# Kernel tuning notes

Hardware: AMD Instinct MI355X
Metric: run time of the kernel (lower is better)

## Reference

```python
import jax, jax.numpy as jnp
import numpy as np


def setup_inputs() -> dict:
    key = jax.random.key(0)
    ks = jax.random.split(key, 4)
    B, M, D = 512, 40, 64
    # split_half=True with layers [200,200,200]: prev = 40 -> 100 -> 100
    x = jax.random.normal(ks[0], (B, M, D), dtype=jnp.float32)
    w1 = jax.random.normal(ks[1], (200, M * 40), dtype=jnp.float32) * 0.02
    w2 = jax.random.normal(ks[2], (200, M * 100), dtype=jnp.float32) * 0.02
    w3 = jax.random.normal(ks[3], (200, M * 100), dtype=jnp.float32) * 0.02
    b1 = jnp.zeros((200,), dtype=jnp.float32)
    b2 = jnp.zeros((200,), dtype=jnp.float32)
    b3 = jnp.zeros((200,), dtype=jnp.float32)
    return {"x": x, "w1": w1, "b1": b1, "w2": w2, "b2": b2, "w3": w3, "b3": b3}


def reference(x, w1, b1, w2, b2, w3, b3):
    B, M, D = x.shape
    params = [(w1, b1), (w2, b2), (w3, b3)]
    n_layers = len(params)
    hidden = x  # (B, prev, D), starts as x0
    outs = []
    for i, (w, b) in enumerate(params):
        # outer product over field dims, flattened channel-major as in torch .view
        outer = jnp.einsum('bmd,bnd->bmnd', x, hidden).reshape(B, -1, D)
        # Conv1d kernel_size=1 == per-position linear over channels
        out = jax.nn.relu(jnp.einsum('bcd,oc->bod', outer, w) + b[None, :, None])
        if i < n_layers - 1:  # split_half
            half = out.shape[1] // 2
            out, direct = out[:, :half, :], out[:, half:, :]
            outs.append(direct)
        else:
            outs.append(out)
        hidden = out
    return jnp.concatenate(outs, axis=1).sum(axis=2)  # (B, 100+100+200)
```

## Files before the change

### kernel.cpp

```cpp
#include <hip/hip_runtime.h>
#include <hip/hip_bf16.h>


typedef float f32x4 __attribute__((ext_vector_type(4)));
typedef short bf16x8 __attribute__((ext_vector_type(8)));
typedef unsigned int uint;

#define XS_STR 44
#define HS_STR 108

struct LDSState {
    __hip_bfloat16 xs[2][64][XS_STR];
    __hip_bfloat16 hs[2][2][64][HS_STR];
    uint U[4][2][64][16];
};

static __device__ __forceinline__ float bflo(uint u) {
    uint v = u << 16; return __builtin_bit_cast(float, v);
}
static __device__ __forceinline__ float bfhi(uint u) {
    uint v = u & 0xffff0000u; return __builtin_bit_cast(float, v);
}
static __device__ __forceinline__ uint pk_bf16(float a, float b) {
    uint r; asm("v_cvt_pk_bf16_f32 %0, %1, %2" : "=v"(r) : "v"(a), "v"(b));
    return r;
}

#define PHASE_BAR() do {                                   \
    asm volatile("s_waitcnt lgkmcnt(0)" ::: "memory");     \
    __builtin_amdgcn_sched_barrier(0);                     \
    __builtin_amdgcn_s_barrier();                          \
    __builtin_amdgcn_sched_barrier(0);                     \
} while (0)

template<int DIV, int NK, int HASH, int ROWLO, int ROWOFF, int HSTR, int A>
__device__ __forceinline__ void layer_core(
    LDSState* L, const bf16x8* __restrict__ wpk, const float* __restrict__ bias,
    const __hip_bfloat16* __restrict__ h0, const __hip_bfloat16* __restrict__ h1,
    int dstpp, float* outb0, float* outb1, int tid, int mt0)
{
    const int lane = tid & 63;
    const int wv = tid >> 6, wn = wv & 1;
    const int q = lane >> 4, lr = lane & 15, d = lane;

    const int hdr = (lr >> 1) & 7;
    const uint* ub  = &L->U[0][0][0][0] + wn * 1024;
    const uint* roA = ub + (lr * 16 + 2 * ((2 * q) ^ hdr));
    const uint* roB = ub + (lr * 16 + 2 * ((2 * q + 1) ^ hdr));

    const int hdw = (d >> 1) & 7;
    uint* wb = &L->U[0][0][d][0] + 2 * (wv ^ hdw);

    const __hip_bfloat16* xb0 = &L->xs[0][d][0];
    const __hip_bfloat16* xb1 = &L->xs[1][d][0];
    const __hip_bfloat16* hb0 = h0 + d * HSTR;
    const __hip_bfloat16* hb1 = h1 + d * HSTR;

    f32x4 acc[A][4];
    #pragma unroll
    for (int mi = 0; mi < A; ++mi)
        #pragma unroll
        for (int nj = 0; nj < 4; ++nj)
            acc[mi][nj] = {0.f, 0.f, 0.f, 0.f};

    int bm = (4 * wv) / DIV;
    int bn = (4 * wv) % DIV;
    int bk = 0;
    auto build = [&]() {
        if (bk < NK) {
            const int slab_dw = (bk & 3) * 2048;
            float xf0 = __bfloat162float(xb0[bm]);
            float xf1 = __bfloat162float(xb1[bm]);
            uint2 ha = *(const uint2*)(hb0 + bn);
            uint2 hc = *(const uint2*)(hb1 + bn);
            uint2 w0, w1;
            w0.x = pk_bf16(xf0 * bflo(ha.x), xf0 * bfhi(ha.x));
            w0.y = pk_bf16(xf0 * bflo(ha.y), xf0 * bfhi(ha.y));
            w1.x = pk_bf16(xf1 * bflo(hc.x), xf1 * bfhi(hc.x));
            w1.y = pk_bf16(xf1 * bflo(hc.y), xf1 * bfhi(hc.y));
            *(uint2*)(wb + slab_dw)        = w0;
            *(uint2*)(wb + slab_dw + 1024) = w1;
            bn += 32;
            if (bn >= DIV) { bn -= DIV; ++bm; }
            ++bk;
        }
    };

    auto prefetch_bv = [&](int s1, bf16x8* bv) {
        const int slab_dw = (s1 & 3) * 2048;
        #pragma unroll
        for (int nj = 0; nj < 4; ++nj) {
            union { uint2 u2[2]; bf16x8 v; } t;
            t.u2[0] = *(const uint2*)(roA + slab_dw + nj * 256);
            t.u2[1] = *(const uint2*)(roB + slab_dw + nj * 256);
            bv[nj] = t.v;
        }
    };

    auto consume_regs = [&](bf16x8* f, bf16x8* bv) {
        #pragma unroll
        for (int mi = 0; mi < A; ++mi)
            #pragma unroll
            for (int nj = 0; nj < 4; ++nj)
                acc[mi][nj] = __builtin_amdgcn_mfma_f32_16x16x32_bf16(
                    f[mi], bv[nj], acc[mi][nj], 0, 0, 0);
    };

    const bf16x8* pw = wpk + (size_t)mt0 * NK * 64 + lane;
    auto loadf = [&](bf16x8* f, int s) {
        if (s < NK) {
            #pragma unroll
            for (int mi = 0; mi < A; ++mi)
                f[mi] = pw[(size_t)mi * NK * 64 + (size_t)s * 64];
        }
    };

    bf16x8 fC[A], fN[A], bvC[4], bvN[4];
    loadf(fC, 0); loadf(fN, 1);
    build(); build();
    __syncthreads();
    prefetch_bv(0, bvC);

    #pragma unroll 1
    for (int s = 0; s + 2 <= NK; s += 2) {
        prefetch_bv(s + 1, bvN);
        consume_regs(fC, bvC);
        loadf(fC, s + 2);
        build();
        PHASE_BAR();
        if (s + 2 < NK) prefetch_bv(s + 2, bvC);
        consume_regs(fN, bvN);
        loadf(fN, s + 3);
        build();
        PHASE_BAR();
    }
    if (NK & 1) consume_regs(fC, bvC);

    float* outp = wn ? outb1 : outb0;
    #pragma unroll
    for (int mi = 0; mi < A; ++mi) {
        const int mt = mt0 + mi;
        #pragma unroll
        for (int reg = 0; reg < 4; ++reg) {
            const int o = 16 * mt + 4 * q + reg;
            if (o < 200) {
                const float bs = bias[o];
                float r0 = fmaxf(acc[mi][0][reg] + bs, 0.f);
                float r1 = fmaxf(acc[mi][1][reg] + bs, 0.f);
                float r2 = fmaxf(acc[mi][2][reg] + bs, 0.f);
                float r3 = fmaxf(acc[mi][3][reg] + bs, 0.f);
                if (HASH && o < 100) {
                    L->hs[dstpp][wn][ 0 + lr][o] = __float2bfloat16(r0);
                    L->hs[dstpp][wn][16 + lr][o] = __float2bfloat16(r1);
                    L->hs[dstpp][wn][32 + lr][o] = __float2bfloat16(r2);
                    L->hs[dstpp][wn][48 + lr][o] = __float2bfloat16(r3);
                }
                if (o >= ROWLO) {
                    float sv = (r0 + r1) + (r2 + r3);
                    sv += __shfl_xor(sv, 1, 64);
                    sv += __shfl_xor(sv, 2, 64);
                    sv += __shfl_xor(sv, 4, 64);
                    sv += __shfl_xor(sv, 8, 64);
                    if (lr == 0) outp[ROWOFF + (o - ROWLO)] = sv;
                }
            }
        }
    }
    __syncthreads();
}

template<int A>
__device__ __forceinline__ void run_layers(
    LDSState* L, const bf16x8* w1p, const bf16x8* w2p, const bf16x8* w3p,
    const float* b1, const float* b2, const float* b3,
    float* outb0, float* outb1, int tid, int mt0)
{
    layer_core< 40,  50, 1, 100,   0, XS_STR, A>(L, w1p, b1,
        &L->xs[0][0][0], &L->xs[1][0][0], 0, outb0, outb1, tid, mt0);
    layer_core<100, 125, 1, 100, 100, HS_STR, A>(L, w2p, b2,
        &L->hs[0][0][0][0], &L->hs[0][1][0][0], 1, outb0, outb1, tid, mt0);
    layer_core<100, 125, 0,   0, 200, HS_STR, A>(L, w3p, b3,
        &L->hs[1][0][0][0], &L->hs[1][1][0][0], 0, outb0, outb1, tid, mt0);
}

__global__ __launch_bounds__(512, 2)
void fused_mfma(const float* __restrict__ x,
                const bf16x8* __restrict__ wpk,
                const float* __restrict__ b1, const float* __restrict__ b2,
                const float* __restrict__ b3, float* __restrict__ out) {
    __shared__ LDSState L;
    const int tid = threadIdx.x;
    const int bi  = blockIdx.x;

    const float* xg = x + (size_t)(2 * bi) * 2560;
    for (int i = tid; i < 5120; i += 512) {
        int bb = (i >= 2560) ? 1 : 0;
        int r  = i - bb * 2560;
        L.xs[bb][r & 63][r >> 6] = __float2bfloat16(xg[(size_t)bb * 2560 + r]);
    }
    __syncthreads();

    float* outb0 = out + (size_t)(2 * bi + 0) * 400;
    float* outb1 = out + (size_t)(2 * bi + 1) * 400;

    const bf16x8* w1p = wpk;
    const bf16x8* w2p = wpk + 41600;
    const bf16x8* w3p = wpk + 145600;

    const int wm = tid >> 7;
    if (wm == 0)
        run_layers<4>(&L, w1p, w2p, w3p, b1, b2, b3, outb0, outb1, tid, 0);
    else
        run_layers<3>(&L, w1p, w2p, w3p, b1, b2, b3, outb0, outb1, tid,
                      3 * wm + 1);
}

__global__ void convert_pack(const float* __restrict__ w1, const float* __restrict__ w2,
                             const float* __restrict__ w3, uint4* __restrict__ outp) {
    int c = blockIdx.x * 256 + threadIdx.x;
    if (c >= 249600) return;
    const float* src; int K, base;
    if (c < 41600)       { src = w1; K = 1600; base = c; }
    else if (c < 145600) { src = w2; K = 4000; base = c - 41600; }
    else                 { src = w3; K = 4000; base = c - 145600; }
    const int NS   = K / 32;
    const int lane = base & 63;
    const int t    = base >> 6;
    const int mt   = t / NS;
    const int s    = t - mt * NS;
    const int row  = 16 * mt + (lane & 15);
    const int k0   = 32 * s + 8 * (lane >> 4);
    uint o[4];
    if (row < 200) {
        const float* p = src + (size_t)row * K + k0;
        #pragma unroll
        for (int j = 0; j < 4; ++j) {
            __hip_bfloat16 lo = __float2bfloat16(p[2 * j]);
            __hip_bfloat16 hi = __float2bfloat16(p[2 * j + 1]);
            o[j] = (uint)__builtin_bit_cast(unsigned short, lo)
                 | ((uint)__builtin_bit_cast(unsigned short, hi) << 16);
        }
    } else {
        #pragma unroll
        for (int j = 0; j < 4; ++j) o[j] = 0u;
    }
    uint4 v; v.x = o[0]; v.y = o[1]; v.z = o[2]; v.w = o[3];
    outp[c] = v;
}

__global__ __launch_bounds__(512, 1)
void fused_bilinear_kernel(const float* __restrict__ x,
                           const float* __restrict__ w1, const float* __restrict__ b1,
                           const float* __restrict__ w2, const float* __restrict__ b2,
                           const float* __restrict__ w3, const float* __restrict__ b3,
                           float* __restrict__ out) {
    const int b   = blockIdx.x;
    const int tid = threadIdx.x;
    const int d   = tid & 63;
    const int wv  = tid >> 6;

    __shared__ float xs[40][64];
    __shared__ float hs[100][64];

    const float* xb = x + (size_t)b * 40 * 64;
    for (int i = tid; i < 40 * 64; i += 512) ((float*)xs)[i] = xb[i];
    __syncthreads();

    float xr[40];
    #pragma unroll
    for (int m = 0; m < 40; ++m) xr[m] = xs[m][d];
    float hr[100];
    const int o0 = __builtin_amdgcn_readfirstlane(wv * 25);

    for (int oi = 0; oi < 25; ++oi) {
        const int o = o0 + oi;
        const float* __restrict__ wrow = w1 + (size_t)o * 1600;
        float s = b1[o];
        for (int m = 0; m < 40; ++m) {
            const float* __restrict__ wm = wrow + m * 40;
            float a0 = 0.f, a1 = 0.f, a2 = 0.f, a3 = 0.f;
            #pragma unroll
            for (int n = 0; n < 40; n += 4) {
                a0 = fmaf(wm[n + 0], xr[n + 0], a0);
                a1 = fmaf(wm[n + 1], xr[n + 1], a1);
                a2 = fmaf(wm[n + 2], xr[n + 2], a2);
                a3 = fmaf(wm[n + 3], xr[n + 3], a3);
            }
            s = fmaf(xs[m][d], (a0 + a1) + (a2 + a3), s);
        }
        s = fmaxf(s, 0.f);
        if (o < 100) hs[o][d] = s;
        else {
            float r = s;
            #pragma unroll
            for (int off = 32; off > 0; off >>= 1) r += __shfl_xor(r, off, 64);
            if (d == 0) out[(size_t)b * 400 + (o - 100)] = r;
        }
    }
    __syncthreads();
    #pragma unroll
    for (int n = 0; n < 100; ++n) hr[n] = hs[n][d];
    __syncthreads();

    for (int oi = 0; oi < 25; ++oi) {
        const int o = o0 + oi;
        const float* __restrict__ wrow = w2 + (size_t)o * 4000;
        float s = b2[o];
        for (int m = 0; m < 40; ++m) {
            const float* __restrict__ wm = wrow + m * 100;
            float a0 = 0.f, a1 = 0.f, a2 = 0.f, a3 = 0.f;
            #pragma unroll
            for (int n = 0; n < 100; n += 4) {
                a0 = fmaf(wm[n + 0], hr[n + 0], a0);
                a1 = fmaf(wm[n + 1], hr[n + 1], a1);
                a2 = fmaf(wm[n + 2], hr[n + 2], a2);
                a3 = fmaf(wm[n + 3], hr[n + 3], a3);
            }
            s = fmaf(xs[m][d], (a0 + a1) + (a2 + a3), s);
        }
        s = fmaxf(s, 0.f);
        if (o < 100) hs[o][d] = s;
        else {
            float r = s;
            #pragma unroll
            for (int off = 32; off > 0; off >>= 1) r += __shfl_xor(r, off, 64);
            if (d == 0) out[(size_t)b * 400 + 100 + (o - 100)] = r;
        }
    }
    __syncthreads();
    #pragma unroll
    for (int n = 0; n < 100; ++n) hr[n] = hs[n][d];

    for (int oi = 0; oi < 25; ++oi) {
        const int o = o0 + oi;
        const float* __restrict__ wrow = w3 + (size_t)o * 4000;
        float s = b3[o];
        for (int m = 0; m < 40; ++m) {
            const float* __restrict__ wm = wrow + m * 100;
            float a0 = 0.f, a1 = 0.f, a2 = 0.f, a3 = 0.f;
            #pragma unroll
            for (int n = 0; n < 100; n += 4) {
                a0 = fmaf(wm[n + 0], hr[n + 0], a0);
                a1 = fmaf(wm[n + 1], hr[n + 1], a1);
                a2 = fmaf(wm[n + 2], hr[n + 2], a2);
                a3 = fmaf(wm[n + 3], hr[n + 3], a3);
            }
            s = fmaf(xs[m][d], (a0 + a1) + (a2 + a3), s);
        }
        s = fmaxf(s, 0.f);
        float r = s;
        #pragma unroll
        for (int off = 32; off > 0; off >>= 1) r += __shfl_xor(r, off, 64);
        if (d == 0) out[(size_t)b * 400 + 200 + o] = r;
    }
}

extern "C" void kernel_launch(void* const* d_in, const int* in_sizes, int n_in,
                              void* d_out, int out_size, void* d_ws, size_t ws_size,
                              hipStream_t stream) {
    const float* x  = (const float*)d_in[0];
    const float* w1 = (const float*)d_in[1];
    const float* b1 = (const float*)d_in[2];
    const float* w2 = (const float*)d_in[3];
    const float* b2 = (const float*)d_in[4];
    const float* w3 = (const float*)d_in[5];
    const float* b3 = (const float*)d_in[6];
    float* out = (float*)d_out;

    if (ws_size >= 249600u * 16u) {
        uint4* wp = (uint4*)d_ws;
        convert_pack<<<dim3(975), dim3(256), 0, stream>>>(w1, w2, w3, wp);
        fused_mfma<<<dim3(256), dim3(512), 0, stream>>>(
            x, (const bf16x8*)wp, b1, b2, b3, out);
    } else {
        fused_bilinear_kernel<<<dim3(512), dim3(512), 0, stream>>>(
            x, w1, b1, w2, b2, w3, b3, out);
    }
}
```

Measured before the change: 186.1 us.

## Deepen LDS slab ring to eight and batch four k-steps per barrier

Doubles the LDS ring of built outer-product slabs from 4 to 8 and restructures the main loop to process four k-slabs between barriers instead of one. It also keeps eight register sets of prefetched weight fragments in flight. The aim is to cut barrier count and expose more memory-level parallelism for the global weight loads. In exchange it uses more LDS and many more VGPRs, which can lower occupancy or cause spills. The remainder handling only covers specific NK%8 values.

```diff
diff --git a/kernel.cpp b/kernel.cpp
--- a/kernel.cpp
+++ b/kernel.cpp
@@ -12,7 +12,7 @@
 struct LDSState {
     __hip_bfloat16 xs[2][64][XS_STR];
     __hip_bfloat16 hs[2][2][64][HS_STR];
-    uint U[4][2][64][16];
+    uint U[8][2][64][16];
 };
 
 static __device__ __forceinline__ float bflo(uint u) {
@@ -68,7 +68,7 @@
     int bk = 0;
     auto build = [&]() {
         if (bk < NK) {
-            const int slab_dw = (bk & 3) * 2048;
+            const int slab_dw = (bk & 7) * 2048;
             float xf0 = __bfloat162float(xb0[bm]);
             float xf1 = __bfloat162float(xb1[bm]);
             uint2 ha = *(const uint2*)(hb0 + bn);
@@ -86,8 +86,8 @@
         }
     };
 
-    auto prefetch_bv = [&](int s1, bf16x8* bv) {
-        const int slab_dw = (s1 & 3) * 2048;
+    auto consume = [&](int slab_dw, bf16x8* f) {
+        bf16x8 bv[4];
         #pragma unroll
         for (int nj = 0; nj < 4; ++nj) {
             union { uint2 u2[2]; bf16x8 v; } t;
@@ -95,9 +95,6 @@
             t.u2[1] = *(const uint2*)(roB + slab_dw + nj * 256);
             bv[nj] = t.v;
         }
-    };
-
-    auto consume_regs = [&](bf16x8* f, bf16x8* bv) {
         #pragma unroll
         for (int mi = 0; mi < A; ++mi)
             #pragma unroll
@@ -115,26 +112,37 @@
         }
     };
 
-    bf16x8 fC[A], fN[A], bvC[4], bvN[4];
-    loadf(fC, 0); loadf(fN, 1);
-    build(); build();
-    __syncthreads();
-    prefetch_bv(0, bvC);
+    bf16x8 a0[A], a1[A], a2[A], a3[A], b0[A], b1[A], b2[A], b3[A];
+    loadf(a0, 0); loadf(a1, 1); loadf(a2, 2); loadf(a3, 3);
+    loadf(b0, 4); loadf(b1, 5); loadf(b2, 6); loadf(b3, 7);
+    build(); build(); build(); build();
+    __syncthreads();
 
     #pragma unroll 1
-    for (int s = 0; s + 2 <= NK; s += 2) {
-        prefetch_bv(s + 1, bvN);
-        consume_regs(fC, bvC);
-        loadf(fC, s + 2);
+    for (int s = 0; s + 8 <= NK; s += 8) {
+        consume(0 * 2048, a0); loadf(a0, s + 8);
+        consume(1 * 2048, a1); loadf(a1, s + 9);
+        consume(2 * 2048, a2); loadf(a2, s + 10);
+        consume(3 * 2048, a3); loadf(a3, s + 11);
+        build(); build(); build(); build();
+        PHASE_BAR();
+        consume(4 * 2048, b0); loadf(b0, s + 12);
+        consume(5 * 2048, b1); loadf(b1, s + 13);
+        consume(6 * 2048, b2); loadf(b2, s + 14);
+        consume(7 * 2048, b3); loadf(b3, s + 15);
+        build(); build(); build(); build();
+        PHASE_BAR();
+    }
+    constexpr int REM = NK % 8;
+    if constexpr (REM >= 1) consume(0 * 2048, a0);
+    if constexpr (REM >= 2) consume(1 * 2048, a1);
+    if constexpr (REM >= 3) consume(2 * 2048, a2);
+    if constexpr (REM >= 4) consume(3 * 2048, a3);
+    if constexpr (REM == 5) {
         build();
         PHASE_BAR();
-        if (s + 2 < NK) prefetch_bv(s + 2, bvC);
-        consume_regs(fN, bvN);
-        loadf(fN, s + 3);
-        build();
-        PHASE_BAR();
-    }
-    if (NK & 1) consume_regs(fC, bvC);
+        consume(4 * 2048, b0);
+    }
 
     float* outp = wn ? outb1 : outb0;
     #pragma unroll
```

Result: faster. 158.7 us, median of 2 (-14.7%).
